# Optimization experiments

Measured on AMD Instinct MI355X. Metric: run time of the kernel, lower is better.

The kernel has to match this reference:

```python
import jax, jax.numpy as jnp
import numpy as np

N0, N1, NB = 247808, 22528, 2048
E0, E1 = 225280, 20480
C = 256
EW = 600000

def setup_inputs() -> dict:
    key = jax.random.key(0)
    ks = jax.random.split(key, 16)
    s = 1.0 / np.sqrt(C)
    return {
        "x": jax.random.normal(ks[0], (N0, C), dtype=jnp.float32),
        "src0": jax.random.randint(ks[1], (E0,), 0, N0),
        "dst0": jax.random.randint(ks[2], (E0,), 0, N1),
        "eid0": jax.random.randint(ks[3], (E0,), 0, EW),
        "src1": jax.random.randint(ks[4], (E1,), 0, N1),
        "dst1": jax.random.randint(ks[5], (E1,), 0, NB),
        "eid1": jax.random.randint(ks[6], (E1,), 0, EW),
        "edge_weight": jax.random.uniform(ks[7], (EW,), dtype=jnp.float32),
        "W_rel0": jax.random.uniform(ks[8], (C, C), jnp.float32, -s, s),
        "b0": jax.random.uniform(ks[9], (C,), jnp.float32, -s, s),
        "W_root0": jax.random.uniform(ks[10], (C, C), jnp.float32, -s, s),
        "W_rel1": jax.random.uniform(ks[11], (C, C), jnp.float32, -s, s),
        "b1": jax.random.uniform(ks[12], (C,), jnp.float32, -s, s),
        "W_root1": jax.random.uniform(ks[13], (C, C), jnp.float32, -s, s),
    }

def graph_conv(x, src, dst, ew, n_dst, W_rel, b, W_root):
    # PyG GraphConv, aggr='mean', bipartite: out_i = W_rel * mean_j(e_ji * x_j) + W_root * x_i + b
    msg = ew[:, None] * x[src]                                   # [E, C]
    agg = jax.ops.segment_sum(msg, dst, num_segments=n_dst)      # [n_dst, C]
    cnt = jax.ops.segment_sum(jnp.ones_like(ew), dst, num_segments=n_dst)
    mean = agg / jnp.maximum(cnt, 1.0)[:, None]
    return mean @ W_rel + b + x[:n_dst] @ W_root

def reference(x, src0, dst0, eid0, src1, dst1, eid1, edge_weight,
              W_rel0, b0, W_root0, W_rel1, b1, W_root1):
    h = graph_conv(x, src0, dst0, edge_weight[eid0], N1, W_rel0, b0, W_root0)
    h = jax.nn.relu(h)  # dropout is identity in eval mode
    h = graph_conv(h, src1, dst1, edge_weight[eid1], NB, W_rel1, b1, W_root1)
    return h, jax.nn.log_softmax(h, axis=1)
```

## Files before the change

kernel.cpp:

```cpp
#include <hip/hip_runtime.h>
#include <cstdint>
#include <cmath>

#define N0c 247808
#define N1c 22528
#define NBc 2048
#define E0c 225280
#define E1c 20480
#define Cc  256
#define NDST (N1c + NBc)
#define ETOT (E0c + E1c)

typedef __attribute__((ext_vector_type(8))) short short8;
typedef __attribute__((ext_vector_type(4))) float floatx4;

__device__ inline unsigned short f2bf(float f) {
    union { float f; unsigned u; } cv; cv.f = f;
    unsigned u = cv.u;
    u += 0x7fffu + ((u >> 16) & 1u);
    return (unsigned short)(u >> 16);
}

__global__ __launch_bounds__(256) void prep_kernel(
    const int* __restrict__ dst0, const int* __restrict__ dst1, int* __restrict__ cnt,
    const float* __restrict__ Wrel0, const float* __restrict__ Wroot0,
    const float* __restrict__ Wrel1, const float* __restrict__ Wroot1,
    short* __restrict__ Wp0, short* __restrict__ Wp1) {
    int b = blockIdx.x;
    if (b < ETOT / 256) {
        int e = b * 256 + threadIdx.x;
        if (e < E0c) atomicAdd(&cnt[dst0[e]], 1);
        else         atomicAdd(&cnt[N1c + dst1[e - E0c]], 1);
    } else {
        int gid = (b - ETOT / 256) * 256 + threadIdx.x;
        int lane = gid & 63;
        int kt = (gid >> 6) & 15;
        int nt = (gid >> 10) & 15;
        int layer = gid >> 14;
        const float* Wrel  = layer ? Wrel1  : Wrel0;
        const float* Wroot = layer ? Wroot1 : Wroot0;
        short* Wp = layer ? Wp1 : Wp0;
        int nn = nt * 16 + (lane & 15);
        int kb = kt * 32 + (lane >> 4) * 8;
        short8 v;
#pragma unroll
        for (int j = 0; j < 8; j++) {
            int k = kb + j;
            float f = (k < 256) ? Wrel[k * 256 + nn] : Wroot[(k - 256) * 256 + nn];
            v[j] = (short)f2bf(f);
        }
        *(short8*)(Wp + (((size_t)nt * 16 + kt) * 64 + lane) * 8) = v;
    }
}

__global__ __launch_bounds__(256) void scan_part(const int* __restrict__ in,
                                                 int* __restrict__ out,
                                                 int* __restrict__ partials) {
    __shared__ int wsum[4];
    int t = threadIdx.x, lane = t & 63, w = t >> 6;
    int base = blockIdx.x * 1024 + t * 4;
    int4 v = *(const int4*)(in + base);
    int s = v.x + v.y + v.z + v.w;
    int incl = s;
#pragma unroll
    for (int o = 1; o < 64; o <<= 1) {
        int u = __shfl_up(incl, o);
        if (lane >= o) incl += u;
    }
    if (lane == 63) wsum[w] = incl;
    __syncthreads();
    int woff = 0;
    for (int j = 0; j < w; j++) woff += wsum[j];
    int excl = woff + incl - s;
    int4 o4;
    o4.x = excl; excl += v.x;
    o4.y = excl; excl += v.y;
    o4.z = excl; excl += v.z;
    o4.w = excl; excl += v.w;
    *(int4*)(out + base) = o4;
    if (t == 255) partials[blockIdx.x] = woff + incl;
}

__global__ __launch_bounds__(256) void scan_add(int* __restrict__ off, int* __restrict__ cur,
                                                const int* __restrict__ partials) {
    __shared__ int pfx_s;
    int t = threadIdx.x;
    if (t < 32) {
        int v = (t < NDST / 1024) ? partials[t] : 0;
        int incl = v;
#pragma unroll
        for (int o = 1; o < 32; o <<= 1) {
            int u = __shfl_up(incl, o);
            if (t >= o) incl += u;
        }
        if (t == (int)blockIdx.x) pfx_s = incl - v;
        if (blockIdx.x == 0 && t == NDST / 1024 - 1) off[NDST] = incl;
    }
    __syncthreads();
    int p = pfx_s;
    int base = blockIdx.x * 1024 + t * 4;
    int4 v = *(const int4*)(off + base);
    v.x += p; v.y += p; v.z += p; v.w += p;
    *(int4*)(off + base) = v;
    *(int4*)(cur + base) = v;
}

__global__ void fill_both(const int* __restrict__ src0, const int* __restrict__ dst0,
                          const int* __restrict__ eid0,
                          const int* __restrict__ src1, const int* __restrict__ dst1,
                          const int* __restrict__ eid1,
                          const float* __restrict__ ew,
                          int* __restrict__ cur, int* __restrict__ srcs,
                          float* __restrict__ wsr) {
    int e = blockIdx.x * blockDim.x + threadIdx.x;
    if (e < E0c) {
        int p = atomicAdd(&cur[dst0[e]], 1);
        srcs[p] = src0[e];
        wsr[p] = ew[eid0[e]];
    } else if (e < ETOT) {
        int i = e - E0c;
        int p = atomicAdd(&cur[N1c + dst1[i]], 1);
        srcs[p] = src1[i];
        wsr[p] = ew[eid1[i]];
    }
}

template <bool ROOT>
__global__ __launch_bounds__(256) void gather_mean_bf16(const float* __restrict__ feat,
                                                        const int* __restrict__ off,
                                                        const int* __restrict__ srcs,
                                                        const float* __restrict__ wsr,
                                                        short* __restrict__ outA,
                                                        int baseRow, int nrows) {
    int wid  = (blockIdx.x * blockDim.x + threadIdx.x) >> 6;
    int lane = threadIdx.x & 63;
    if (wid >= nrows) return;
    int crow = baseRow + wid;
    int s = off[crow], e = off[crow + 1];
    float4 acc = make_float4(0.f, 0.f, 0.f, 0.f);
    int i = s;
    for (; i + 3 < e; i += 4) {
        int   s0 = srcs[i],     s1 = srcs[i + 1], s2 = srcs[i + 2], s3 = srcs[i + 3];
        float w0 = wsr[i],      w1 = wsr[i + 1],  w2 = wsr[i + 2],  w3 = wsr[i + 3];
        float4 v0 = ((const float4*)(feat + (size_t)s0 * Cc))[lane];
        float4 v1 = ((const float4*)(feat + (size_t)s1 * Cc))[lane];
        float4 v2 = ((const float4*)(feat + (size_t)s2 * Cc))[lane];
        float4 v3 = ((const float4*)(feat + (size_t)s3 * Cc))[lane];
        acc.x += w0 * v0.x + w1 * v1.x + w2 * v2.x + w3 * v3.x;
        acc.y += w0 * v0.y + w1 * v1.y + w2 * v2.y + w3 * v3.y;
        acc.z += w0 * v0.z + w1 * v1.z + w2 * v2.z + w3 * v3.z;
        acc.w += w0 * v0.w + w1 * v1.w + w2 * v2.w + w3 * v3.w;
    }
    for (; i < e; i++) {
        int sid = srcs[i];
        float w = wsr[i];
        float4 v = ((const float4*)(feat + (size_t)sid * Cc))[lane];
        acc.x += w * v.x; acc.y += w * v.y; acc.z += w * v.z; acc.w += w * v.w;
    }
    float inv = 1.0f / fmaxf((float)(e - s), 1.0f);
    ushort4 o;
    o.x = f2bf(acc.x * inv); o.y = f2bf(acc.y * inv);
    o.z = f2bf(acc.z * inv); o.w = f2bf(acc.w * inv);
    *(ushort4*)(outA + (size_t)wid * 512 + lane * 4) = o;
    if (ROOT) {
        float4 r = ((const float4*)(feat + (size_t)crow * Cc))[lane];
        ushort4 ro;
        ro.x = f2bf(r.x); ro.y = f2bf(r.y); ro.z = f2bf(r.z); ro.w = f2bf(r.w);
        *(ushort4*)(outA + (size_t)wid * 512 + 256 + lane * 4) = ro;
    }
}

template <bool RELU, bool EXTRA, bool SMAX>
__global__ __launch_bounds__(256) void gemm_mfma(const short* __restrict__ A,
                                                 const short* __restrict__ Wp,
                                                 const float* __restrict__ bias,
                                                 float* __restrict__ out,
                                                 short* __restrict__ extra,
                                                 float* __restrict__ out1) {
    __shared__ short As[32 * 520];
    int t = threadIdx.x;
    int base = blockIdx.x * 32;
#pragma unroll
    for (int it = 0; it < 8; it++) {
        int idx = it * 256 + t;
        int row = idx >> 6, c = idx & 63;
        short8 v = *(const short8*)(A + (size_t)(base + row) * 512 + c * 8);
        *(short8*)(&As[row * 520 + c * 8]) = v;
    }
    __syncthreads();

    int lane = t & 63, w = t >> 6;
    int l15 = lane & 15, lq = lane >> 4;
    floatx4 acc[2][4];
#pragma unroll
    for (int rt = 0; rt < 2; rt++)
#pragma unroll
        for (int ct = 0; ct < 4; ct++) acc[rt][ct] = (floatx4){0.f, 0.f, 0.f, 0.f};

    for (int kt = 0; kt < 16; kt++) {
        short8 a0 = *(const short8*)(&As[l15 * 520 + kt * 32 + lq * 8]);
        short8 a1 = *(const short8*)(&As[(16 + l15) * 520 + kt * 32 + lq * 8]);
#pragma unroll
        for (int ct = 0; ct < 4; ct++) {
            int nt = w * 4 + ct;
            short8 b = *(const short8*)(Wp + (((size_t)nt * 16 + kt) * 64 + lane) * 8);
            acc[0][ct] = __builtin_amdgcn_mfma_f32_16x16x32_bf16(a0, b, acc[0][ct], 0, 0, 0);
            acc[1][ct] = __builtin_amdgcn_mfma_f32_16x16x32_bf16(a1, b, acc[1][ct], 0, 0, 0);
        }
    }

    float* Ls = (float*)As;
    if (SMAX) __syncthreads();

#pragma unroll
    for (int rt = 0; rt < 2; rt++)
#pragma unroll
        for (int ct = 0; ct < 4; ct++) {
            int col = (w * 4 + ct) * 16 + l15;
            float bv = bias[col];
#pragma unroll
            for (int r = 0; r < 4; r++) {
                int rl = rt * 16 + lq * 4 + r;
                int row = base + rl;
                float val = acc[rt][ct][r] + bv;
                if (RELU) val = fmaxf(val, 0.f);
                out[(size_t)row * Cc + col] = val;
                if (EXTRA) {
                    if (row < NBc) extra[(size_t)row * 512 + 256 + col] = (short)f2bf(val);
                }
                if (SMAX) Ls[rl * 260 + col] = val;
            }
        }

    if (SMAX) {
        __syncthreads();
        for (int rr = 0; rr < 8; rr++) {
            int rl = w * 8 + rr;
            float4 v = *(const float4*)(Ls + rl * 260 + lane * 4);
            float m = fmaxf(fmaxf(v.x, v.y), fmaxf(v.z, v.w));
#pragma unroll
            for (int o = 32; o; o >>= 1) m = fmaxf(m, __shfl_xor(m, o));
            float s = expf(v.x - m) + expf(v.y - m) + expf(v.z - m) + expf(v.w - m);
#pragma unroll
            for (int o = 32; o; o >>= 1) s += __shfl_xor(s, o);
            float lse = m + logf(s);
            float4 o4;
            o4.x = v.x - lse; o4.y = v.y - lse; o4.z = v.z - lse; o4.w = v.w - lse;
            *(float4*)(out1 + (size_t)(base + rl) * Cc + lane * 4) = o4;
        }
    }
}

extern "C" void kernel_launch(void* const* d_in, const int* in_sizes, int n_in,
                              void* d_out, int out_size, void* d_ws, size_t ws_size,
                              hipStream_t stream) {
    const float* x     = (const float*)d_in[0];
    const int*   src0  = (const int*)d_in[1];
    const int*   dst0  = (const int*)d_in[2];
    const int*   eid0  = (const int*)d_in[3];
    const int*   src1  = (const int*)d_in[4];
    const int*   dst1  = (const int*)d_in[5];
    const int*   eid1  = (const int*)d_in[6];
    const float* ew    = (const float*)d_in[7];
    const float* Wrel0 = (const float*)d_in[8];
    const float* b0    = (const float*)d_in[9];
    const float* Wroot0= (const float*)d_in[10];
    const float* Wrel1 = (const float*)d_in[11];
    const float* b1    = (const float*)d_in[12];
    const float* Wroot1= (const float*)d_in[13];

    char* wsb = (char*)d_ws;
    size_t o = 0;
    auto alloc = [&](size_t bytes) { void* p = wsb + o; o += (bytes + 15) & ~(size_t)15; return p; };
    int*   off   = (int*)  alloc((NDST + 1) * 4);
    int*   cnt   = (int*)  alloc(NDST * 4);
    int*   srcs  = (int*)  alloc(ETOT * 4);
    float* wsr   = (float*)alloc(ETOT * 4);
    int*   parts = (int*)  alloc(64 * 4);
    short* Wp0   = (short*)alloc(16 * 16 * 64 * 8 * 2);
    short* Wp1   = (short*)alloc(16 * 16 * 64 * 8 * 2);
    short* A0    = (short*)alloc((size_t)N1c * 512 * 2);
    short* A1    = (short*)alloc((size_t)NBc * 512 * 2);
    float* h     = (float*)alloc((size_t)N1c * Cc * 4);

    hipMemsetAsync(cnt, 0, NDST * sizeof(int), stream);
    prep_kernel<<<ETOT / 256 + 128, 256, 0, stream>>>(dst0, dst1, cnt,
                                                      Wrel0, Wroot0, Wrel1, Wroot1, Wp0, Wp1);
    scan_part<<<NDST / 1024, 256, 0, stream>>>(cnt, off, parts);
    scan_add<<<NDST / 1024, 256, 0, stream>>>(off, cnt, parts);
    fill_both<<<ETOT / 256, 256, 0, stream>>>(src0, dst0, eid0, src1, dst1, eid1,
                                              ew, cnt, srcs, wsr);

    gather_mean_bf16<true><<<(N1c * 64) / 256, 256, 0, stream>>>(x, off, srcs, wsr, A0, 0, N1c);
    gemm_mfma<true, true, false><<<N1c / 32, 256, 0, stream>>>(A0, Wp0, b0, h, A1, nullptr);

    gather_mean_bf16<false><<<(NBc * 64) / 256, 256, 0, stream>>>(h, off, srcs, wsr, A1, N1c, NBc);
    float* out2 = (float*)d_out;
    gemm_mfma<false, false, true><<<NBc / 32, 256, 0, stream>>>(A1, Wp1, b1, out2, nullptr,
                                                                out2 + (size_t)NBc * Cc);
}
```

Measured before the change: 443.3 us.

## Fuse neighbor gather-mean into MFMA GEMM via shared memory, pack edge src/weight

Merges the gather-mean kernel and the bf16 MFMA GEMM into one kernel per layer. Each block gathers its 32 destination rows straight into shared memory and then runs the GEMM, so the intermediate A0/A1 bf16 buffers are never written to or read from global memory. Edge source index and weight are packed into a single int2 array so each edge needs one load. The cost is less parallelism in the gather phase: each wave now handles 8 rows in sequence, with fewer blocks, and the GEMM cannot start until the slowest row in its block finishes.

```diff
diff --git a/kernel.cpp b/kernel.cpp
--- a/kernel.cpp
+++ b/kernel.cpp
@@ -110,92 +110,75 @@
                           const int* __restrict__ src1, const int* __restrict__ dst1,
                           const int* __restrict__ eid1,
                           const float* __restrict__ ew,
-                          int* __restrict__ cur, int* __restrict__ srcs,
-                          float* __restrict__ wsr) {
+                          int* __restrict__ cur, int2* __restrict__ epk) {
     int e = blockIdx.x * blockDim.x + threadIdx.x;
     if (e < E0c) {
         int p = atomicAdd(&cur[dst0[e]], 1);
-        srcs[p] = src0[e];
-        wsr[p] = ew[eid0[e]];
+        epk[p] = make_int2(src0[e], __float_as_int(ew[eid0[e]]));
     } else if (e < ETOT) {
         int i = e - E0c;
         int p = atomicAdd(&cur[N1c + dst1[i]], 1);
-        srcs[p] = src1[i];
-        wsr[p] = ew[eid1[i]];
-    }
-}
-
-template <bool ROOT>
-__global__ __launch_bounds__(256) void gather_mean_bf16(const float* __restrict__ feat,
-                                                        const int* __restrict__ off,
-                                                        const int* __restrict__ srcs,
-                                                        const float* __restrict__ wsr,
-                                                        short* __restrict__ outA,
-                                                        int baseRow, int nrows) {
-    int wid  = (blockIdx.x * blockDim.x + threadIdx.x) >> 6;
-    int lane = threadIdx.x & 63;
-    if (wid >= nrows) return;
-    int crow = baseRow + wid;
-    int s = off[crow], e = off[crow + 1];
-    float4 acc = make_float4(0.f, 0.f, 0.f, 0.f);
-    int i = s;
-    for (; i + 3 < e; i += 4) {
-        int   s0 = srcs[i],     s1 = srcs[i + 1], s2 = srcs[i + 2], s3 = srcs[i + 3];
-        float w0 = wsr[i],      w1 = wsr[i + 1],  w2 = wsr[i + 2],  w3 = wsr[i + 3];
-        float4 v0 = ((const float4*)(feat + (size_t)s0 * Cc))[lane];
-        float4 v1 = ((const float4*)(feat + (size_t)s1 * Cc))[lane];
-        float4 v2 = ((const float4*)(feat + (size_t)s2 * Cc))[lane];
-        float4 v3 = ((const float4*)(feat + (size_t)s3 * Cc))[lane];
-        acc.x += w0 * v0.x + w1 * v1.x + w2 * v2.x + w3 * v3.x;
-        acc.y += w0 * v0.y + w1 * v1.y + w2 * v2.y + w3 * v3.y;
-        acc.z += w0 * v0.z + w1 * v1.z + w2 * v2.z + w3 * v3.z;
-        acc.w += w0 * v0.w + w1 * v1.w + w2 * v2.w + w3 * v3.w;
-    }
-    for (; i < e; i++) {
-        int sid = srcs[i];
-        float w = wsr[i];
-        float4 v = ((const float4*)(feat + (size_t)sid * Cc))[lane];
-        acc.x += w * v.x; acc.y += w * v.y; acc.z += w * v.z; acc.w += w * v.w;
-    }
-    float inv = 1.0f / fmaxf((float)(e - s), 1.0f);
-    ushort4 o;
-    o.x = f2bf(acc.x * inv); o.y = f2bf(acc.y * inv);
-    o.z = f2bf(acc.z * inv); o.w = f2bf(acc.w * inv);
-    *(ushort4*)(outA + (size_t)wid * 512 + lane * 4) = o;
-    if (ROOT) {
-        float4 r = ((const float4*)(feat + (size_t)crow * Cc))[lane];
+        epk[p] = make_int2(src1[i], __float_as_int(ew[eid1[i]]));
+    }
+}
+
+template <bool RELU, bool SMAX>
+__global__ __launch_bounds__(256, 4) void fused_layer(
+        const float* __restrict__ feat,
+        const int*  __restrict__ off,
+        const int2* __restrict__ epk,
+        const short* __restrict__ Wp,
+        const float* __restrict__ bias,
+        float* __restrict__ out,
+        float* __restrict__ out1,
+        int baseRow) {
+    __shared__ short As[32 * 520];
+    int t = threadIdx.x, lane = t & 63, w = t >> 6;
+    int base = blockIdx.x * 32;
+
+    for (int rr = 0; rr < 8; rr++) {
+        int rl = w * 8 + rr;
+        int row = base + rl;
+        int s = off[baseRow + row], e = off[baseRow + row + 1];
+        float4 acc = make_float4(0.f, 0.f, 0.f, 0.f);
+        int i = s;
+        for (; i + 3 < e; i += 4) {
+            int2 e0 = epk[i], e1 = epk[i + 1], e2 = epk[i + 2], e3 = epk[i + 3];
+            float w0 = __int_as_float(e0.y), w1 = __int_as_float(e1.y);
+            float w2 = __int_as_float(e2.y), w3 = __int_as_float(e3.y);
+            float4 v0 = ((const float4*)(feat + (size_t)e0.x * Cc))[lane];
+            float4 v1 = ((const float4*)(feat + (size_t)e1.x * Cc))[lane];
+            float4 v2 = ((const float4*)(feat + (size_t)e2.x * Cc))[lane];
+            float4 v3 = ((const float4*)(feat + (size_t)e3.x * Cc))[lane];
+            acc.x += w0 * v0.x + w1 * v1.x + w2 * v2.x + w3 * v3.x;
+            acc.y += w0 * v0.y + w1 * v1.y + w2 * v2.y + w3 * v3.y;
+            acc.z += w0 * v0.z + w1 * v1.z + w2 * v2.z + w3 * v3.z;
+            acc.w += w0 * v0.w + w1 * v1.w + w2 * v2.w + w3 * v3.w;
+        }
+        for (; i < e; i++) {
+            int2 ee = epk[i];
+            float wt = __int_as_float(ee.y);
+            float4 v = ((const float4*)(feat + (size_t)ee.x * Cc))[lane];
+            acc.x += wt * v.x; acc.y += wt * v.y; acc.z += wt * v.z; acc.w += wt * v.w;
+        }
+        float inv = 1.0f / fmaxf((float)(e - s), 1.0f);
+        ushort4 o;
+        o.x = f2bf(acc.x * inv); o.y = f2bf(acc.y * inv);
+        o.z = f2bf(acc.z * inv); o.w = f2bf(acc.w * inv);
+        *(ushort4*)(&As[rl * 520 + lane * 4]) = o;
+        float4 r = ((const float4*)(feat + (size_t)row * Cc))[lane];
         ushort4 ro;
         ro.x = f2bf(r.x); ro.y = f2bf(r.y); ro.z = f2bf(r.z); ro.w = f2bf(r.w);
-        *(ushort4*)(outA + (size_t)wid * 512 + 256 + lane * 4) = ro;
-    }
-}
-
-template <bool RELU, bool EXTRA, bool SMAX>
-__global__ __launch_bounds__(256) void gemm_mfma(const short* __restrict__ A,
-                                                 const short* __restrict__ Wp,
-                                                 const float* __restrict__ bias,
-                                                 float* __restrict__ out,
-                                                 short* __restrict__ extra,
-                                                 float* __restrict__ out1) {
-    __shared__ short As[32 * 520];
-    int t = threadIdx.x;
-    int base = blockIdx.x * 32;
-#pragma unroll
-    for (int it = 0; it < 8; it++) {
-        int idx = it * 256 + t;
-        int row = idx >> 6, c = idx & 63;
-        short8 v = *(const short8*)(A + (size_t)(base + row) * 512 + c * 8);
-        *(short8*)(&As[row * 520 + c * 8]) = v;
+        *(ushort4*)(&As[rl * 520 + 256 + lane * 4]) = ro;
     }
     __syncthreads();
 
-    int lane = t & 63, w = t >> 6;
     int l15 = lane & 15, lq = lane >> 4;
-    floatx4 acc[2][4];
+    floatx4 accg[2][4];
 #pragma unroll
     for (int rt = 0; rt < 2; rt++)
 #pragma unroll
-        for (int ct = 0; ct < 4; ct++) acc[rt][ct] = (floatx4){0.f, 0.f, 0.f, 0.f};
+        for (int ct = 0; ct < 4; ct++) accg[rt][ct] = (floatx4){0.f, 0.f, 0.f, 0.f};
 
     for (int kt = 0; kt < 16; kt++) {
         short8 a0 = *(const short8*)(&As[l15 * 520 + kt * 32 + lq * 8]);
@@ -204,8 +187,8 @@
         for (int ct = 0; ct < 4; ct++) {
             int nt = w * 4 + ct;
             short8 b = *(const short8*)(Wp + (((size_t)nt * 16 + kt) * 64 + lane) * 8);
-            acc[0][ct] = __builtin_amdgcn_mfma_f32_16x16x32_bf16(a0, b, acc[0][ct], 0, 0, 0);
-            acc[1][ct] = __builtin_amdgcn_mfma_f32_16x16x32_bf16(a1, b, acc[1][ct], 0, 0, 0);
+            accg[0][ct] = __builtin_amdgcn_mfma_f32_16x16x32_bf16(a0, b, accg[0][ct], 0, 0, 0);
+            accg[1][ct] = __builtin_amdgcn_mfma_f32_16x16x32_bf16(a1, b, accg[1][ct], 0, 0, 0);
         }
     }
 
@@ -222,12 +205,9 @@
             for (int r = 0; r < 4; r++) {
                 int rl = rt * 16 + lq * 4 + r;
                 int row = base + rl;
-                float val = acc[rt][ct][r] + bv;
+                float val = accg[rt][ct][r] + bv;
                 if (RELU) val = fmaxf(val, 0.f);
                 out[(size_t)row * Cc + col] = val;
-                if (EXTRA) {
-                    if (row < NBc) extra[(size_t)row * 512 + 256 + col] = (short)f2bf(val);
-                }
                 if (SMAX) Ls[rl * 260 + col] = val;
             }
         }
@@ -274,13 +254,10 @@
     auto alloc = [&](size_t bytes) { void* p = wsb + o; o += (bytes + 15) & ~(size_t)15; return p; };
     int*   off   = (int*)  alloc((NDST + 1) * 4);
     int*   cnt   = (int*)  alloc(NDST * 4);
-    int*   srcs  = (int*)  alloc(ETOT * 4);
-    float* wsr   = (float*)alloc(ETOT * 4);
+    int2*  epk   = (int2*) alloc((size_t)ETOT * 8);
     int*   parts = (int*)  alloc(64 * 4);
     short* Wp0   = (short*)alloc(16 * 16 * 64 * 8 * 2);
     short* Wp1   = (short*)alloc(16 * 16 * 64 * 8 * 2);
-    short* A0    = (short*)alloc((size_t)N1c * 512 * 2);
-    short* A1    = (short*)alloc((size_t)NBc * 512 * 2);
     float* h     = (float*)alloc((size_t)N1c * Cc * 4);
 
     hipMemsetAsync(cnt, 0, NDST * sizeof(int), stream);
@@ -289,13 +266,12 @@
     scan_part<<<NDST / 1024, 256, 0, stream>>>(cnt, off, parts);
     scan_add<<<NDST / 1024, 256, 0, stream>>>(off, cnt, parts);
     fill_both<<<ETOT / 256, 256, 0, stream>>>(src0, dst0, eid0, src1, dst1, eid1,
-                                              ew, cnt, srcs, wsr);
-
-    gather_mean_bf16<true><<<(N1c * 64) / 256, 256, 0, stream>>>(x, off, srcs, wsr, A0, 0, N1c);
-    gemm_mfma<true, true, false><<<N1c / 32, 256, 0, stream>>>(A0, Wp0, b0, h, A1, nullptr);
-
-    gather_mean_bf16<false><<<(NBc * 64) / 256, 256, 0, stream>>>(h, off, srcs, wsr, A1, N1c, NBc);
+                                              ew, cnt, epk);
+
+    fused_layer<true, false><<<N1c / 32, 256, 0, stream>>>(x, off, epk, Wp0, b0,
+                                                           h, nullptr, 0);
+
     float* out2 = (float*)d_out;
-    gemm_mfma<false, false, true><<<NBc / 32, 256, 0, stream>>>(A1, Wp1, b1, out2, nullptr,
-                                                                out2 + (size_t)NBc * Cc);
-}
+    fused_layer<false, true><<<NBc / 32, 256, 0, stream>>>(h, off, epk, Wp1, b1,
+                                                           out2, out2 + (size_t)NBc * Cc, N1c);
+}
```

Result: no change. 443.5 us (+0.0%).
